# Kernel tuning notes

Hardware: AMD Instinct MI355X
Metric: run time of the kernel (lower is better)

Reference implementation:

```python
import jax, jax.numpy as jnp
import numpy as np

N_NODES = 100000
N_EDGES = 1600000
IN_CH = 24
OUT_CH = 128


def _linear_params(key, fan_in, fan_out):
    k1, k2 = jax.random.split(key)
    s = 1.0 / np.sqrt(fan_in)
    w = jax.random.uniform(k1, (fan_in, fan_out), jnp.float32, -s, s)
    b = jax.random.uniform(k2, (fan_out,), jnp.float32, -s, s)
    return w, b


def setup_inputs() -> dict:
    key = jax.random.key(0)
    ks = jax.random.split(key, 10)
    x = jax.random.normal(ks[0], (N_NODES, IN_CH), jnp.float32)
    edge_index = jax.random.randint(ks[1], (2, N_EDGES), 0, N_NODES, jnp.int64)
    w1a, b1a = _linear_params(ks[2], 2 * IN_CH, OUT_CH)
    w1b, b1b = _linear_params(ks[3], OUT_CH, OUT_CH)
    w2a, b2a = _linear_params(ks[4], 2 * OUT_CH, OUT_CH)
    w2b, b2b = _linear_params(ks[5], OUT_CH, OUT_CH)
    w3a, b3a = _linear_params(ks[6], 2 * OUT_CH, OUT_CH)
    w3b, b3b = _linear_params(ks[7], OUT_CH, OUT_CH)
    fw, fb = _linear_params(ks[8], 16, 1)
    return dict(x=x, edge_index=edge_index,
                w1a=w1a, b1a=b1a, w1b=w1b, b1b=b1b,
                w2a=w2a, b2a=b2a, w2b=w2b, b2b=b2b,
                w3a=w3a, b3a=b3a, w3b=w3b, b3b=b3b,
                fw=fw, fb=fb)


def _edge_conv(x, src, dst, wa, ba, wb, bb):
    # gather endpoints: x_i = target, x_j = source (PyG convention)
    x_i = x[dst]
    x_j = x[src]
    tmp = jnp.concatenate([x_i, x_j - x_i], axis=1)        # [E, 2*C]
    msg = jax.nn.relu(tmp @ wa + ba) @ wb + bb             # [E, out]
    agg = jax.ops.segment_max(msg, dst, num_segments=N_NODES)
    # PyG max-aggr yields 0 for nodes with no incoming edges
    return jnp.where(jnp.isneginf(agg), 0.0, agg)


def reference(x, edge_index, w1a, b1a, w1b, b1b, w2a, b2a, w2b, b2b,
              w3a, b3a, w3b, b3b, fw, fb):
    src = edge_index[0]
    dst = edge_index[1]
    x2 = jax.nn.relu(_edge_conv(x, src, dst, w1a, b1a, w1b, b1b))
    x4 = jax.nn.relu(_edge_conv(x2, src, dst, w2a, b2a, w2b, b2b))
    x6 = jax.nn.relu(_edge_conv(x4, src, dst, w3a, b3a, w3b, b3b))
    x7 = jnp.concatenate([x2, x4, x6], axis=1)             # [N, 3*OUT_CH]
    # MaxPool1d(kernel=IN_CH, stride=IN_CH) over last dim: 384 -> 16
    x8 = x7.reshape(N_NODES, 3 * OUT_CH // IN_CH, IN_CH).max(axis=-1)
    return x8 @ fw + fb                                     # [N, 1]
```

## Files before the change

### kernel.cpp

```cpp
#include <hip/hip_runtime.h>
#include <stdint.h>

#define NN 100000
#define NE 1600000
#define MAXD 64

using short8 = __attribute__((ext_vector_type(8))) short;
using f32x4  = __attribute__((ext_vector_type(4))) float;
typedef unsigned short ushort_t;

__device__ __forceinline__ ushort_t f2bf(float f){
  union { float f; uint32_t u; } v; v.f = f;
  uint32_t u = v.u;
  uint32_t r = (u + 0x7fffu + ((u >> 16) & 1u)) >> 16;
  return (ushort_t)r;
}
__device__ __forceinline__ float bf2f(ushort_t h){
  union { uint32_t u; float f; } v; v.u = ((uint32_t)h) << 16;
  return v.f;
}

__global__ void k_detect(const unsigned* ei, int* flag){
  __shared__ int any;
  if(threadIdx.x == 0) any = 0;
  __syncthreads();
  unsigned w = ei[2*threadIdx.x + 1];
  if(w) atomicOr(&any, 1);
  __syncthreads();
  if(threadIdx.x == 0) *flag = (any == 0) ? 1 : 0;
}

__global__ void k_build(const int* ei, const int* flag, int* cursor, int* list){
  int e = blockIdx.x * blockDim.x + threadIdx.x;
  if(e >= NE) return;
  bool i64 = (*flag != 0);
  int src, dst;
  if(i64){
    const long long* p = (const long long*)ei;
    src = (int)p[e]; dst = (int)p[NE + e];
  } else {
    src = ei[e]; dst = ei[NE + e];
  }
  if((unsigned)src >= NN || (unsigned)dst >= NN) return;
  int pos = atomicAdd(&cursor[dst], 1);
  if(pos < MAXD) list[dst*MAXD + pos] = src;
}

__global__ void k_wcatfrag(const float* wa, ushort_t* dst, int C, int KT){
  int idx = blockIdx.x*blockDim.x + threadIdx.x;
  int total = 16*KT*64*8;
  if(idx >= total) return;
  int j = idx & 7, lane = (idx>>3)&63;
  int rest = idx >> 9;
  int kt = rest % KT, nt = rest / KT;
  int k = kt*32 + ((lane>>4)<<3) + j;
  int n = nt*16 + (lane & 15);
  float v = 0.f;
  if(k < C) v = (n < 128) ? (wa[k*128+n] - wa[(C+k)*128+n]) : wa[(C+k)*128 + (n-128)];
  dst[idx] = f2bf(v);
}

__global__ void k_wbfrag(const float* wb, ushort_t* dst){
  int idx = blockIdx.x*blockDim.x + threadIdx.x;
  if(idx >= 8*4*64*8) return;
  int j = idx & 7, lane = (idx>>3)&63;
  int kt = (idx>>9)&3, nt = idx>>11;
  int k = kt*32 + ((lane>>4)<<3) + j;
  int n = nt*16 + (lane & 15);
  dst[idx] = f2bf(wb[k*128 + n]);
}

template<int KT, int ROWLEN, bool SPLIT>
__global__ __launch_bounds__(256)
void k_gemm(const void* xin_, const ushort_t* __restrict__ wfrag,
            const float* __restrict__ bias, float* __restrict__ Atab,
            ushort_t* __restrict__ Btab)
{
  constexpr int K  = KT*32;
  constexpr int RB = K*2 + 16;
  __shared__ ushort_t shHi[64*RB/2];
  __shared__ ushort_t shLo[SPLIT ? 64*RB/2 : 2];

  const int t = threadIdx.x;
  const int wave = t >> 6, lane = t & 63;
  const int l15 = lane & 15, lg = lane >> 4;

  short8 bf[4][KT];
  #pragma unroll
  for(int ntl=0; ntl<4; ntl++)
    #pragma unroll
    for(int kt=0; kt<KT; kt++){
      int nt = wave*4 + ntl;
      bf[ntl][kt] = *(const short8*)&wfrag[((nt*KT + kt)*64 + lane)*8];
    }
  float bv[4] = {0.f,0.f,0.f,0.f};
  if(wave < 2){
    #pragma unroll
    for(int ntl=0; ntl<4; ntl++) bv[ntl] = bias[wave*64 + ntl*16 + l15];
  }

  const int row0 = blockIdx.x * 64;

  constexpr int GROUPS = 64*(K/8);
  #pragma unroll
  for(int it=0; it<GROUPS/256; it++){
    int gi  = t + it*256;
    int row = gi / (K/8), kg = gi % (K/8);
    int gr  = row0 + row;
    int off = (row*RB + kg*16) >> 1;
    if constexpr (SPLIT){
      const float* xin = (const float*)xin_;
      short8 hi8, lo8;
      #pragma unroll
      for(int j=0;j<8;j++){
        int k = kg*8 + j;
        float v = (gr < NN && k < ROWLEN) ? xin[(size_t)gr*ROWLEN + k] : 0.f;
        ushort_t h = f2bf(v);
        hi8[j] = (short)h;
        lo8[j] = (short)f2bf(v - bf2f(h));
      }
      *(short8*)&shHi[off] = hi8;
      *(short8*)&shLo[off] = lo8;
    } else {
      const ushort_t* xb = (const ushort_t*)xin_;
      short8 h8 = {0,0,0,0,0,0,0,0};
      if(gr < NN) h8 = *(const short8*)&xb[(size_t)gr*ROWLEN + kg*8];
      *(short8*)&shHi[off] = h8;
    }
  }
  __syncthreads();

  #pragma unroll
  for(int mc=0; mc<4; mc++){
    f32x4 acc[4];
    #pragma unroll
    for(int ntl=0; ntl<4; ntl++) acc[ntl] = (f32x4){0.f,0.f,0.f,0.f};
    #pragma unroll
    for(int kt=0; kt<KT; kt++){
      int off = ((mc*16 + l15)*RB + kt*64 + lg*16) >> 1;
      short8 ah = *(const short8*)&shHi[off];
      #pragma unroll
      for(int ntl=0; ntl<4; ntl++)
        acc[ntl] = __builtin_amdgcn_mfma_f32_16x16x32_bf16(ah, bf[ntl][kt], acc[ntl], 0,0,0);
      if constexpr (SPLIT){
        short8 al = *(const short8*)&shLo[off];
        #pragma unroll
        for(int ntl=0; ntl<4; ntl++)
          acc[ntl] = __builtin_amdgcn_mfma_f32_16x16x32_bf16(al, bf[ntl][kt], acc[ntl], 0,0,0);
      }
    }
    #pragma unroll
    for(int ntl=0; ntl<4; ntl++){
      #pragma unroll
      for(int q=0; q<4; q++){
        int gr = row0 + mc*16 + lg*4 + q;
        if(gr < NN){
          if(wave < 2){
            int ch = wave*64 + ntl*16 + l15;
            Atab[(size_t)gr*128 + ch] = acc[ntl][q] + bv[ntl];
          } else {
            int ch = (wave-2)*64 + ntl*16 + l15;
            Btab[(size_t)gr*128 + ch] = f2bf(acc[ntl][q]);
          }
        }
      }
    }
  }
}

template<bool F32OUT>
__global__ __launch_bounds__(256)
void k_edge(const float* __restrict__ Atab, const ushort_t* __restrict__ Btab,
            const ushort_t* __restrict__ wbfrag, const float* __restrict__ bias2,
            const int* __restrict__ deg, const int* __restrict__ list,
            float* __restrict__ outF, ushort_t* __restrict__ outB)
{
  __shared__ float    shA[128];
  __shared__ ushort_t shH[16*272/2];

  const int t = threadIdx.x;
  const int wave = t >> 6, lane = t & 63;
  const int l15 = lane & 15, lg = lane >> 4;
  const int eg  = t >> 4;
  const int ch8 = (t & 15) * 8;

  short8 wf[2][4];
  #pragma unroll
  for(int ntl=0; ntl<2; ntl++)
    #pragma unroll
    for(int kt=0; kt<4; kt++){
      int nt = wave*2 + ntl;
      wf[ntl][kt] = *(const short8*)&wbfrag[((nt*4 + kt)*64 + lane)*8];
    }
  float bbv[2];
  #pragma unroll
  for(int ntl=0; ntl<2; ntl++) bbv[ntl] = bias2[wave*32 + ntl*16 + l15];

  for(int n = blockIdx.x; n < NN; n += gridDim.x){
    int d = deg[n]; if(d > MAXD) d = MAXD;
    if(d == 0){
      if(lane < 16){
        #pragma unroll
        for(int ntl=0; ntl<2; ntl++){
          int ch = wave*32 + ntl*16 + lane;
          if(F32OUT) outF[(size_t)n*128 + ch] = 0.f;
          else       outB[(size_t)n*128 + ch] = 0;
        }
      }
      continue;
    }
    __syncthreads();
    if(t < 128) shA[t] = Atab[(size_t)n*128 + t];
    __syncthreads();

    float m0 = -3.0e38f, m1 = -3.0e38f;
    const int* lst = &list[(size_t)n*MAXD];
    int nch = (d + 15) >> 4;
    for(int c = 0; c < nch; c++){
      int ei = c*16 + eg; if(ei >= d) ei = d - 1;
      int s = lst[ei];
      short8 bvv = *(const short8*)&Btab[(size_t)s*128 + ch8];
      short8 hw;
      #pragma unroll
      for(int j=0;j<8;j++){
        float h = shA[ch8 + j] + bf2f((ushort_t)bvv[j]);
        h = h > 0.f ? h : 0.f;
        hw[j] = (short)f2bf(h);
      }
      __syncthreads();
      *(short8*)&shH[(eg*272 + (t&15)*16) >> 1] = hw;
      __syncthreads();

      f32x4 macc0 = (f32x4){0.f,0.f,0.f,0.f};
      f32x4 macc1 = (f32x4){0.f,0.f,0.f,0.f};
      #pragma unroll
      for(int kt=0; kt<4; kt++){
        short8 a = *(const short8*)&shH[(l15*272 + kt*64 + lg*16) >> 1];
        macc0 = __builtin_amdgcn_mfma_f32_16x16x32_bf16(a, wf[0][kt], macc0, 0,0,0);
        macc1 = __builtin_amdgcn_mfma_f32_16x16x32_bf16(a, wf[1][kt], macc1, 0,0,0);
      }
      float mm0 = fmaxf(fmaxf(macc0[0],macc0[1]), fmaxf(macc0[2],macc0[3]));
      mm0 = fmaxf(mm0, __shfl_xor(mm0, 16, 64));
      mm0 = fmaxf(mm0, __shfl_xor(mm0, 32, 64));
      m0  = fmaxf(m0, mm0);
      float mm1 = fmaxf(fmaxf(macc1[0],macc1[1]), fmaxf(macc1[2],macc1[3]));
      mm1 = fmaxf(mm1, __shfl_xor(mm1, 16, 64));
      mm1 = fmaxf(mm1, __shfl_xor(mm1, 32, 64));
      m1  = fmaxf(m1, mm1);
    }
    if(lane < 16){
      float v0 = fmaxf(m0 + bbv[0], 0.f);
      float v1 = fmaxf(m1 + bbv[1], 0.f);
      int ch = wave*32 + lane;
      if(F32OUT){
        outF[(size_t)n*128 + ch]      = v0;
        outF[(size_t)n*128 + ch + 16] = v1;
      } else {
        outB[(size_t)n*128 + ch]      = f2bf(v0);
        outB[(size_t)n*128 + ch + 16] = f2bf(v1);
      }
    }
  }
}

template<bool F32IN>
__global__ __launch_bounds__(256)
void k_final(const void* x2_, const void* x4_, const void* x6_,
             const float* __restrict__ fw, const float* __restrict__ fb,
             float* __restrict__ out)
{
  __shared__ float arr[4][384];
  int wave = threadIdx.x >> 6, lane = threadIdx.x & 63;
  int n = blockIdx.x*4 + wave;
  if(n < NN){
    const void* xs[3] = {x2_, x4_, x6_};
    #pragma unroll
    for(int tt=0; tt<3; tt++){
      float a, b;
      if(F32IN){
        const float* p = (const float*)xs[tt] + (size_t)n*128 + lane*2;
        a = p[0]; b = p[1];
      } else {
        const ushort_t* p = (const ushort_t*)xs[tt] + (size_t)n*128 + lane*2;
        a = bf2f(p[0]); b = bf2f(p[1]);
      }
      arr[wave][tt*128 + lane*2]     = a;
      arr[wave][tt*128 + lane*2 + 1] = b;
    }
  }
  __syncthreads();
  if(n < NN && lane < 16){
    float m = -3.0e38f;
    #pragma unroll
    for(int j=0;j<24;j++) m = fmaxf(m, arr[wave][lane*24 + j]);
    float p = m * fw[lane];
    #pragma unroll
    for(int off=1; off<16; off<<=1) p += __shfl_xor(p, off, 64);
    if(lane == 0) out[n] = p + fb[0];
  }
}

extern "C" void kernel_launch(void* const* d_in, const int* in_sizes, int n_in,
                              void* d_out, int out_size, void* d_ws, size_t ws_size,
                              hipStream_t stream)
{
  const float* x   = (const float*)d_in[0];
  const void*  ei  = d_in[1];
  const float* w1a = (const float*)d_in[2];
  const float* b1a = (const float*)d_in[3];
  const float* w1b = (const float*)d_in[4];
  const float* b1b = (const float*)d_in[5];
  const float* w2a = (const float*)d_in[6];
  const float* b2a = (const float*)d_in[7];
  const float* w2b = (const float*)d_in[8];
  const float* b2b = (const float*)d_in[9];
  const float* w3a = (const float*)d_in[10];
  const float* b3a = (const float*)d_in[11];
  const float* w3b = (const float*)d_in[12];
  const float* b3b = (const float*)d_in[13];
  const float* fw  = (const float*)d_in[14];
  const float* fb  = (const float*)d_in[15];

  char* ws = (char*)d_ws;
  size_t off = 0;
  auto alloc = [&](size_t bytes) -> void* {
    void* p = ws + off;
    off = (off + bytes + 255) & ~(size_t)255;
    return p;
  };
  int*      flag   = (int*)alloc(4);
  int*      cursor = (int*)alloc((size_t)NN*4);
  int*      list   = (int*)alloc((size_t)NN*MAXD*4);
  float*    Atab   = (float*)alloc((size_t)NN*128*4);
  ushort_t* Btab   = (ushort_t*)alloc((size_t)NN*128*2);
  ushort_t* wf1    = (ushort_t*)alloc(16*1*64*8*2);
  ushort_t* wf2    = (ushort_t*)alloc(16*4*64*8*2);
  ushort_t* wf3    = (ushort_t*)alloc(16*4*64*8*2);
  ushort_t* wbf1   = (ushort_t*)alloc(8*4*64*8*2);
  ushort_t* wbf2   = (ushort_t*)alloc(8*4*64*8*2);
  ushort_t* wbf3   = (ushort_t*)alloc(8*4*64*8*2);

  size_t fixed = off;
  bool planA = (ws_size >= fixed + 3*(size_t)NN*128*4 + 1024);
  void *x2, *x4, *x6;
  size_t xbytes = planA ? (size_t)NN*128*4 : (size_t)NN*128*2;
  x2 = alloc(xbytes); x4 = alloc(xbytes); x6 = alloc(xbytes);

  hipMemsetAsync(cursor, 0, (size_t)NN*4, stream);
  k_detect<<<1, 128, 0, stream>>>((const unsigned*)ei, flag);
  k_build<<<(NE + 255)/256, 256, 0, stream>>>((const int*)ei, flag, cursor, list);

  k_wcatfrag<<<(16*1*64*8 + 255)/256, 256, 0, stream>>>(w1a, wf1, 24, 1);
  k_wcatfrag<<<(16*4*64*8 + 255)/256, 256, 0, stream>>>(w2a, wf2, 128, 4);
  k_wcatfrag<<<(16*4*64*8 + 255)/256, 256, 0, stream>>>(w3a, wf3, 128, 4);
  k_wbfrag<<<64, 256, 0, stream>>>(w1b, wbf1);
  k_wbfrag<<<64, 256, 0, stream>>>(w2b, wbf2);
  k_wbfrag<<<64, 256, 0, stream>>>(w3b, wbf3);

  const int GT = (NN + 63)/64;
  const int EG = 4096;

  k_gemm<1,24,true><<<GT, 256, 0, stream>>>(x, wf1, b1a, Atab, Btab);
  if(planA){
    k_edge<true><<<EG, 256, 0, stream>>>(Atab, Btab, wbf1, b1b, cursor, list, (float*)x2, nullptr);
    k_gemm<4,128,true><<<GT, 256, 0, stream>>>(x2, wf2, b2a, Atab, Btab);
    k_edge<true><<<EG, 256, 0, stream>>>(Atab, Btab, wbf2, b2b, cursor, list, (float*)x4, nullptr);
    k_gemm<4,128,true><<<GT, 256, 0, stream>>>(x4, wf3, b3a, Atab, Btab);
    k_edge<true><<<EG, 256, 0, stream>>>(Atab, Btab, wbf3, b3b, cursor, list, (float*)x6, nullptr);
    k_final<true><<<(NN + 3)/4, 256, 0, stream>>>(x2, x4, x6, fw, fb, (float*)d_out);
  } else {
    k_edge<false><<<EG, 256, 0, stream>>>(Atab, Btab, wbf1, b1b, cursor, list, nullptr, (ushort_t*)x2);
    k_gemm<4,128,false><<<GT, 256, 0, stream>>>(x2, wf2, b2a, Atab, Btab);
    k_edge<false><<<EG, 256, 0, stream>>>(Atab, Btab, wbf2, b2b, cursor, list, nullptr, (ushort_t*)x4);
    k_gemm<4,128,false><<<GT, 256, 0, stream>>>(x4, wf3, b3a, Atab, Btab);
    k_edge<false><<<EG, 256, 0, stream>>>(Atab, Btab, wbf3, b3b, cursor, list, nullptr, (ushort_t*)x6);
    k_final<false><<<(NN + 3)/4, 256, 0, stream>>>(x2, x4, x6, fw, fb, (float*)d_out);
  }
}
```

Baseline: 857.4 us.

## Double-buffer edge tile in LDS, prefetch next gather, defer max reduction

The edge kernel now double-buffers its LDS hidden tile, which removes one of the two block barriers per 16-edge chunk. It also prefetches the next chunk's gathered Btab row before the barrier so the load overlaps the MFMA work. The per-node A row is read straight into registers instead of going through shared memory, and bf16 packing uses the hardware v_cvt_pk_bf16_f32 instruction. The cross-lane max shuffles move out of the chunk loop and run once per node, at the cost of more registers for the prefetch and per-lane accumulators.

```diff
diff --git a/kernel.cpp b/kernel.cpp
--- a/kernel.cpp
+++ b/kernel.cpp
@@ -7,6 +7,7 @@
 
 using short8 = __attribute__((ext_vector_type(8))) short;
 using f32x4  = __attribute__((ext_vector_type(4))) float;
+using u32x4  = __attribute__((ext_vector_type(4))) unsigned int;
 typedef unsigned short ushort_t;
 
 __device__ __forceinline__ ushort_t f2bf(float f){
@@ -175,14 +176,13 @@
             const int* __restrict__ deg, const int* __restrict__ list,
             float* __restrict__ outF, ushort_t* __restrict__ outB)
 {
-  __shared__ float    shA[128];
-  __shared__ ushort_t shH[16*272/2];
+  __shared__ ushort_t shH[2][16*272/2];
 
   const int t = threadIdx.x;
   const int wave = t >> 6, lane = t & 63;
   const int l15 = lane & 15, lg = lane >> 4;
   const int eg  = t >> 4;
-  const int ch8 = (t & 15) * 8;
+  const int cg  = t & 15;
 
   short8 wf[2][4];
   #pragma unroll
@@ -196,6 +196,7 @@
   #pragma unroll
   for(int ntl=0; ntl<2; ntl++) bbv[ntl] = bias2[wave*32 + ntl*16 + l15];
 
+  int buf = 0;
   for(int n = blockIdx.x; n < NN; n += gridDim.x){
     int d = deg[n]; if(d > MAXD) d = MAXD;
     if(d == 0){
@@ -209,48 +210,67 @@
       }
       continue;
     }
-    __syncthreads();
-    if(t < 128) shA[t] = Atab[(size_t)n*128 + t];
-    __syncthreads();
-
-    float m0 = -3.0e38f, m1 = -3.0e38f;
     const int* lst = &list[(size_t)n*MAXD];
+    const float4* ap = (const float4*)&Atab[(size_t)n*128 + cg*8];
+    float4 a0 = ap[0], a1 = ap[1];
+    float af[8] = {a0.x,a0.y,a0.z,a0.w,a1.x,a1.y,a1.z,a1.w};
+
+    f32x4 mac0 = (f32x4){-3.0e38f,-3.0e38f,-3.0e38f,-3.0e38f};
+    f32x4 mac1 = mac0;
+
     int nch = (d + 15) >> 4;
+    int ei0 = (eg < d) ? eg : d - 1;
+    short8 b8 = *(const short8*)&Btab[(size_t)lst[ei0]*128 + cg*8];
+
     for(int c = 0; c < nch; c++){
-      int ei = c*16 + eg; if(ei >= d) ei = d - 1;
-      int s = lst[ei];
-      short8 bvv = *(const short8*)&Btab[(size_t)s*128 + ch8];
-      short8 hw;
-      #pragma unroll
-      for(int j=0;j<8;j++){
-        float h = shA[ch8 + j] + bf2f((ushort_t)bvv[j]);
-        h = h > 0.f ? h : 0.f;
-        hw[j] = (short)f2bf(h);
-      }
+      union { short8 s; uint32_t u[4]; } bb; bb.s = b8;
+      u32x4 pkv;
+      #pragma unroll
+      for(int p=0; p<4; p++){
+        uint32_t w = bb.u[p];
+        float flo = __uint_as_float(w << 16);
+        float fhi = __uint_as_float(w & 0xffff0000u);
+        float hlo = fmaxf(af[2*p]   + flo, 0.f);
+        float hhi = fmaxf(af[2*p+1] + fhi, 0.f);
+        uint32_t pw;
+        asm("v_cvt_pk_bf16_f32 %0, %1, %2" : "=v"(pw) : "v"(hlo), "v"(hhi));
+        pkv[p] = pw;
+      }
+      *(u32x4*)&shH[buf][(eg*272 + cg*16) >> 1] = pkv;
+
+      if(c + 1 < nch){
+        int e2 = (c+1)*16 + eg; if(e2 >= d) e2 = d - 1;
+        b8 = *(const short8*)&Btab[(size_t)lst[e2]*128 + cg*8];
+      }
+
       __syncthreads();
-      *(short8*)&shH[(eg*272 + (t&15)*16) >> 1] = hw;
-      __syncthreads();
-
-      f32x4 macc0 = (f32x4){0.f,0.f,0.f,0.f};
-      f32x4 macc1 = (f32x4){0.f,0.f,0.f,0.f};
+
+      f32x4 acc0 = (f32x4){0.f,0.f,0.f,0.f};
+      f32x4 acc1 = (f32x4){0.f,0.f,0.f,0.f};
       #pragma unroll
       for(int kt=0; kt<4; kt++){
-        short8 a = *(const short8*)&shH[(l15*272 + kt*64 + lg*16) >> 1];
-        macc0 = __builtin_amdgcn_mfma_f32_16x16x32_bf16(a, wf[0][kt], macc0, 0,0,0);
-        macc1 = __builtin_amdgcn_mfma_f32_16x16x32_bf16(a, wf[1][kt], macc1, 0,0,0);
-      }
-      float mm0 = fmaxf(fmaxf(macc0[0],macc0[1]), fmaxf(macc0[2],macc0[3]));
-      mm0 = fmaxf(mm0, __shfl_xor(mm0, 16, 64));
-      mm0 = fmaxf(mm0, __shfl_xor(mm0, 32, 64));
-      m0  = fmaxf(m0, mm0);
-      float mm1 = fmaxf(fmaxf(macc1[0],macc1[1]), fmaxf(macc1[2],macc1[3]));
-      mm1 = fmaxf(mm1, __shfl_xor(mm1, 16, 64));
-      mm1 = fmaxf(mm1, __shfl_xor(mm1, 32, 64));
-      m1  = fmaxf(m1, mm1);
-    }
+        short8 a = *(const short8*)&shH[buf][(l15*272 + kt*64 + lg*16) >> 1];
+        acc0 = __builtin_amdgcn_mfma_f32_16x16x32_bf16(a, wf[0][kt], acc0, 0,0,0);
+        acc1 = __builtin_amdgcn_mfma_f32_16x16x32_bf16(a, wf[1][kt], acc1, 0,0,0);
+      }
+      #pragma unroll
+      for(int q=0; q<4; q++){
+        mac0[q] = fmaxf(mac0[q], acc0[q]);
+        mac1[q] = fmaxf(mac1[q], acc1[q]);
+      }
+      buf ^= 1;
+    }
+
+    float mm0 = fmaxf(fmaxf(mac0[0],mac0[1]), fmaxf(mac0[2],mac0[3]));
+    mm0 = fmaxf(mm0, __shfl_xor(mm0, 16, 64));
+    mm0 = fmaxf(mm0, __shfl_xor(mm0, 32, 64));
+    float mm1 = fmaxf(fmaxf(mac1[0],mac1[1]), fmaxf(mac1[2],mac1[3]));
+    mm1 = fmaxf(mm1, __shfl_xor(mm1, 16, 64));
+    mm1 = fmaxf(mm1, __shfl_xor(mm1, 32, 64));
+
     if(lane < 16){
-      float v0 = fmaxf(m0 + bbv[0], 0.f);
-      float v1 = fmaxf(m1 + bbv[1], 0.f);
+      float v0 = fmaxf(mm0 + bbv[0], 0.f);
+      float v1 = fmaxf(mm1 + bbv[1], 0.f);
       int ch = wave*32 + lane;
       if(F32OUT){
         outF[(size_t)n*128 + ch]      = v0;
```

Result: no change. 842.0 us (-1.8%).
